# Performance work log

Measured on AMD Instinct MI355X. Metric: run time of the kernel, lower is better.

Reference implementation:

```python
import jax, jax.numpy as jnp
import numpy as np
from jax import lax

B, N, C, FH, FW = 2, 6, 64, 16, 44
D = 64
DEPTH_MIN, DEPTH_MAX = 1.0, 60.0
IMG_H, IMG_W = 256, 704
BEV_H, BEV_W = 128, 128
XMIN, XMAX = -51.2, 51.2
YMIN, YMAX = -51.2, 51.2
BN_EPS = 1e-5


def _make_cameras():
    fx = fy = 557.0
    K = np.array([[fx, 0.0, IMG_W / 2.0], [0.0, fy, IMG_H / 2.0], [0.0, 0.0, 1.0]], np.float32)
    intr = np.broadcast_to(K, (B, N, 3, 3)).copy()
    extr = np.zeros((B, N, 4, 4), np.float32)
    for n in range(N):
        c, s = np.cos(2 * np.pi * n / N), np.sin(2 * np.pi * n / N)
        # columns = [right, down, forward] of camera expressed in ego frame
        Rc = np.array([[s, 0.0, c], [-c, 0.0, s], [0.0, -1.0, 0.0]], np.float32)
        extr[:, n, :3, :3] = Rc
        extr[:, n, :3, 3] = np.array([c, s, 1.5], np.float32)
        extr[:, n, 3, 3] = 1.0
    return jnp.asarray(intr), jnp.asarray(extr)


def _frustum():
    # (D, FH, FW, 3) holding (u*d, v*d, d) in original-image pixel coords
    ds = jnp.linspace(DEPTH_MIN, DEPTH_MAX, D)[:, None, None]
    xs = jnp.linspace(0.0, IMG_W - 1.0, FW)[None, None, :]
    ys = jnp.linspace(0.0, IMG_H - 1.0, FH)[None, :, None]
    d = jnp.broadcast_to(ds, (D, FH, FW))
    x = jnp.broadcast_to(xs, (D, FH, FW))
    y = jnp.broadcast_to(ys, (D, FH, FW))
    return jnp.stack([x * d, y * d, d], axis=-1)


def _conv(x, w, b, pad):
    y = lax.conv_general_dilated(x, w, (1, 1), pad, dimension_numbers=("NCHW", "OIHW", "NCHW"))
    return y + b[None, :, None, None]


def setup_inputs() -> dict:
    key = jax.random.key(0)
    k0, k1, k2 = jax.random.split(key, 3)
    intr, extr = _make_cameras()
    return {
        "features": jax.random.normal(k0, (B, N, C, FH, FW), jnp.float32),
        "intrinsics": intr,
        "extrinsics": extr,
        "conv1_w": jax.random.normal(k1, (C, C, 3, 3), jnp.float32) / np.sqrt(C * 9.0).astype(np.float32),
        "conv1_b": jnp.zeros((C,), jnp.float32),
        "bn_gamma": jnp.ones((C,), jnp.float32),
        "bn_beta": jnp.zeros((C,), jnp.float32),
        "bn_mean": jnp.zeros((C,), jnp.float32),
        "bn_var": jnp.ones((C,), jnp.float32),
        "conv2_w": jax.random.normal(k2, (D, C, 1, 1), jnp.float32) / np.sqrt(float(C)).astype(np.float32),
        "conv2_b": jnp.zeros((D,), jnp.float32),
    }


def reference(features, intrinsics, extrinsics, conv1_w, conv1_b, bn_gamma, bn_beta, bn_mean, bn_var, conv2_w, conv2_b):
    Bv, Nv, Cv, fH, fW = features.shape
    x = features.reshape(Bv * Nv, Cv, fH, fW)

    # DepthNet: conv3x3 -> BN (inference form) -> ReLU -> conv1x1 -> softmax over depth bins
    h = _conv(x, conv1_w, conv1_b, "SAME")
    scale = (bn_gamma / jnp.sqrt(bn_var + BN_EPS))[None, :, None, None]
    h = (h - bn_mean[None, :, None, None]) * scale + bn_beta[None, :, None, None]
    h = jax.nn.relu(h)
    depth = jax.nn.softmax(_conv(h, conv2_w, conv2_b, "VALID"), axis=1)  # (B*N, D, fH, fW)

    # Lift: outer product of features with depth distribution
    volume = x[:, :, None] * depth[:, None]  # (B*N, C, D, fH, fW)

    # Unproject frustum to ego frame for every camera
    pts = _frustum()  # (D, fH, fW, 3)
    Kinv = jnp.linalg.inv(intrinsics)  # (B, N, 3, 3)
    cam = jnp.einsum("bnij,dhwj->bndhwi", Kinv, pts)
    R = extrinsics[..., :3, :3]
    t = extrinsics[..., :3, 3]
    ego = jnp.einsum("bnij,bndhwj->bndhwi", R, cam) + t[:, :, None, None, None, :]

    # BEV voxel indices; invalid points routed to an overflow bucket that is dropped
    ix = jnp.floor((ego[..., 0] - XMIN) / (XMAX - XMIN) * BEV_W).astype(jnp.int32)
    iy = jnp.floor((ego[..., 1] - YMIN) / (YMAX - YMIN) * BEV_H).astype(jnp.int32)
    valid = (ix >= 0) & (ix < BEV_W) & (iy >= 0) & (iy < BEV_H)
    idx = jnp.where(valid, iy * BEV_W + ix, BEV_H * BEV_W)  # (B, N, D, fH, fW)

    # Splat: scatter-add over all cameras/depths/pixels per batch element
    vol = volume.reshape(Bv, Nv, Cv, -1).transpose(0, 2, 1, 3).reshape(Bv, Cv, -1)  # (B, C, N*D*fH*fW)
    idxb = idx.reshape(Bv, -1)

    def pool(v, i):
        return jnp.zeros((Cv, BEV_H * BEV_W + 1), v.dtype).at[:, i].add(v)[:, :-1]

    return jax.vmap(pool)(vol, idxb).reshape(Bv, Cv, BEV_H, BEV_W)
```

## Files before the change

kernel.cpp:

```cpp
#include <hip/hip_runtime.h>
#include <hip/hip_bf16.h>
#include <math.h>

#define B_  2
#define N_  6
#define C_  64
#define FH_ 16
#define FW_ 44
#define D_  64
#define PIX (FH_*FW_)
#define BNI (B_*N_)
#define NPILLAR (BNI*PIX)
#define NPOINT (NPILLAR*D_)
#define BEVH 128
#define BEVW 128
#define BEVC (BEVH*BEVW)
#define NCELL (B_*BEVC)
#define PW 46
#define PP (18*PW)

typedef unsigned int u32;

__device__ __forceinline__ int rlane_i(int v, int l) {
    return __builtin_amdgcn_readlane(v, l);
}
__device__ __forceinline__ float rlane_f(float v, int l) {
    return __int_as_float(__builtin_amdgcn_readlane(__float_as_int(v), l));
}

__global__ __launch_bounds__(256) void k_init_conv(const float* __restrict__ feat,
                                                   const float* __restrict__ w1,
                                                   float* __restrict__ hpAll,
                                                   float* __restrict__ x_t,
                                                   const float* __restrict__ w2,
                                                   float* __restrict__ w2t,
                                                   u32* __restrict__ counts,
                                                   u32* __restrict__ gcursor,
                                                   const float* __restrict__ intr,
                                                   const float* __restrict__ extr,
                                                   double* __restrict__ Mbuf) {
    const int blk = blockIdx.x;
    const int tid = threadIdx.x;

    __shared__ float smem[16 * PP];

    if (blk < 768) {
        if (blk < 128) counts[blk * 256 + tid] = 0u;

        const int bn = blk >> 6;
        const int ch = (blk >> 4) & 3;
        const int o0 = (blk & 15) * 4;
        const int c0 = ch * 16;

        for (int t = tid; t < 4 * PP; t += 256)
            ((float4*)smem)[t] = make_float4(0.f, 0.f, 0.f, 0.f);
        __syncthreads();

        const float4* fb4 = (const float4*)(feat + ((size_t)bn * C_ + c0) * PIX);
#pragma unroll
        for (int k = 0; k < 11; ++k) {
            const int j = k * 256 + tid;
            const int pl = j / 176;
            const int r  = j % 176;
            const int row = r / 11, q = r % 11;
            const float4 v = fb4[j];
            float* dstp = &smem[pl * PP + (row + 1) * PW + q * 4 + 1];
            dstp[0] = v.x; dstp[1] = v.y; dstp[2] = v.z; dstp[3] = v.w;
        }
        __syncthreads();

        const int y0 = tid / FW_,          x0 = tid % FW_;
        const int y1 = (tid + 256) / FW_,  x1 = (tid + 256) % FW_;
        const int y2 = (tid + 512) / FW_,  x2 = (tid + 512) % FW_;
        const int rp0 = y0 * PW + x0;
        const int rp1 = y1 * PW + x1;
        const int rp2 = y2 * PW + x2;

        float a00=0,a01=0,a02=0,a03=0, a10=0,a11=0,a12=0,a13=0,
              a20=0,a21=0,a22=0,a23=0;
#pragma unroll 4
        for (int i = 0; i < 16; ++i) {
            const float* wr0 = w1 + ((size_t)(o0 + 0) * C_ + c0 + i) * 9;
            const float* wr1 = w1 + ((size_t)(o0 + 1) * C_ + c0 + i) * 9;
            const float* wr2 = w1 + ((size_t)(o0 + 2) * C_ + c0 + i) * 9;
            const float* wr3 = w1 + ((size_t)(o0 + 3) * C_ + c0 + i) * 9;
            const float* pb = &smem[i * PP];
#define CONV_SLOT(RP, A0, A1, A2, A3)                                          \
    {                                                                          \
        const float* bb = pb + (RP);                                           \
        const float n0=bb[0], n1=bb[1], n2=bb[2];                              \
        const float n3=bb[PW], n4=bb[PW+1], n5=bb[PW+2];                       \
        const float n6=bb[2*PW], n7=bb[2*PW+1], n8=bb[2*PW+2];                 \
        A0 += n0*wr0[0]+n1*wr0[1]+n2*wr0[2]+n3*wr0[3]+n4*wr0[4]                \
            + n5*wr0[5]+n6*wr0[6]+n7*wr0[7]+n8*wr0[8];                         \
        A1 += n0*wr1[0]+n1*wr1[1]+n2*wr1[2]+n3*wr1[3]+n4*wr1[4]                \
            + n5*wr1[5]+n6*wr1[6]+n7*wr1[7]+n8*wr1[8];                         \
        A2 += n0*wr2[0]+n1*wr2[1]+n2*wr2[2]+n3*wr2[3]+n4*wr2[4]                \
            + n5*wr2[5]+n6*wr2[6]+n7*wr2[7]+n8*wr2[8];                         \
        A3 += n0*wr3[0]+n1*wr3[1]+n2*wr3[2]+n3*wr3[3]+n4*wr3[4]                \
            + n5*wr3[5]+n6*wr3[6]+n7*wr3[7]+n8*wr3[8];                         \
    }
            CONV_SLOT(rp0, a00, a01, a02, a03);
            CONV_SLOT(rp1, a10, a11, a12, a13);
            if (tid < PIX - 512) CONV_SLOT(rp2, a20, a21, a22, a23);
#undef CONV_SLOT
        }
        float* hp = hpAll + (size_t)ch * NPOINT + (size_t)bn * PIX * C_;
        *(float4*)&hp[(size_t)tid * C_ + o0]         = make_float4(a00,a01,a02,a03);
        *(float4*)&hp[(size_t)(tid + 256) * C_ + o0] = make_float4(a10,a11,a12,a13);
        if (tid < PIX - 512)
            *(float4*)&hp[(size_t)(tid + 512) * C_ + o0] = make_float4(a20,a21,a22,a23);
    } else if (blk < 900) {
        const int u  = blk - 768;
        const int bn = u / 11;
        const int p0 = (u % 11) * 64;
        const int lane = tid & 63;
        const int row4 = tid >> 6;
        float* tile = smem;
#pragma unroll
        for (int k = 0; k < 16; ++k) {
            const int c = k * 4 + row4;
            tile[c * 65 + lane] = feat[((size_t)bn * C_ + c) * PIX + p0 + lane];
        }
        __syncthreads();
#pragma unroll
        for (int k = 0; k < 16; ++k) {
            const int r = k * 4 + row4;
            x_t[((size_t)bn * PIX + p0 + r) * C_ + lane] = tile[lane * 65 + r];
        }
    } else {
#pragma unroll
        for (int k = 0; k < 16; ++k) {
            const int idx = k * 256 + tid;
            const int d = idx >> 6, c = idx & 63;
            w2t[c * D_ + d] = w2[idx];
        }
        if (tid == 0) *gcursor = 0u;
        if (tid < BNI) {
            const float* K = &intr[tid * 9];
            const double a00 = K[0], a01 = K[1], a02 = K[2];
            const double a10 = K[3], a11 = K[4], a12 = K[5];
            const double a20 = K[6], a21 = K[7], a22 = K[8];
            const double det = a00 * (a11 * a22 - a12 * a21)
                             - a01 * (a10 * a22 - a12 * a20)
                             + a02 * (a10 * a21 - a11 * a20);
            const double id = 1.0 / det;
            double inv[9];
            inv[0] = (a11 * a22 - a12 * a21) * id;
            inv[1] = (a02 * a21 - a01 * a22) * id;
            inv[2] = (a01 * a12 - a02 * a11) * id;
            inv[3] = (a12 * a20 - a10 * a22) * id;
            inv[4] = (a00 * a22 - a02 * a20) * id;
            inv[5] = (a02 * a10 - a00 * a12) * id;
            inv[6] = (a10 * a21 - a11 * a20) * id;
            inv[7] = (a01 * a20 - a00 * a21) * id;
            inv[8] = (a00 * a11 - a01 * a10) * id;
            const float* E = &extr[tid * 16];
            double* M = &Mbuf[tid * 9];
            for (int r = 0; r < 3; ++r) {
                const double r0 = E[r*4+0], r1 = E[r*4+1], r2 = E[r*4+2];
                M[r*3+0] = r0*inv[0] + r1*inv[3] + r2*inv[6];
                M[r*3+1] = r0*inv[1] + r1*inv[4] + r2*inv[7];
                M[r*3+2] = r0*inv[2] + r1*inv[5] + r2*inv[8];
            }
        }
    }
}

__global__ __launch_bounds__(256) void k_depth(const float* __restrict__ hpAll,
                                               const float* __restrict__ b1,
                                               const float* __restrict__ gma,
                                               const float* __restrict__ bta,
                                               const float* __restrict__ mu,
                                               const float* __restrict__ var,
                                               const float* __restrict__ w2t,
                                               const float* __restrict__ b2,
                                               const double* __restrict__ Mbuf,
                                               const float* __restrict__ extr,
                                               uint2* __restrict__ pc,
                                               u32* __restrict__ counts) {
    const int wv = threadIdx.x >> 6;
    const int d  = threadIdx.x & 63;
    const int pillar = blockIdx.x * 4 + wv;
    const int bn = pillar / PIX;
    const int p  = pillar % PIX;
    const int yi = p / FW_;
    const int xi = p % FW_;

    __shared__ float hs[4][C_];
    {
        const size_t o = (size_t)pillar * C_ + d;
        float h = hpAll[o] + hpAll[NPOINT + o] + hpAll[2 * (size_t)NPOINT + o]
                + hpAll[3 * (size_t)NPOINT + o] + b1[d];
        const float sc = gma[d] / sqrtf(var[d] + 1e-5f);
        h = (h - mu[d]) * sc + bta[d];
        hs[wv][d] = h > 0.f ? h : 0.f;
    }
    __syncthreads();

    float logit = b2[d];
#pragma unroll
    for (int c = 0; c < C_; ++c) logit += hs[wv][c] * w2t[c * D_ + d];

    float m = logit;
#pragma unroll
    for (int off = 32; off; off >>= 1) m = fmaxf(m, __shfl_xor(m, off));
    float e = expf(logit - m);
    float s = e;
#pragma unroll
    for (int off = 32; off; off >>= 1) s += __shfl_xor(s, off);

    const double* M = &Mbuf[bn * 9];
    const double xn = (double)xi * (703.0 / 43.0);
    const double yn = (double)yi * 17.0;
    const double vx = M[0] * xn + M[1] * yn + M[2];
    const double vy = M[3] * xn + M[4] * yn + M[5];
    const double dd = 1.0 + (double)d * (59.0 / 63.0);
    const float* E = &extr[bn * 16];
    const double ex = dd * vx + (double)E[3];
    const double ey = dd * vy + (double)E[7];
    const int ix = (int)floor((ex + 51.2) * 1.25);
    const int iy = (int)floor((ey + 51.2) * 1.25);
    const bool valid = (ix >= 0) && (ix < BEVW) && (iy >= 0) && (iy < BEVH);

    const int i = pillar * D_ + d;
    uint2 rec;
    rec.x = __float_as_uint(e / s);
    if (valid) {
        const int cell = (bn / N_) * BEVC + iy * BEVW + ix;
        const u32 rank = atomicAdd(&counts[cell], 1u);
        rec.y = (rank << 15) | (u32)cell;
    } else {
        rec.y = 0xFFFFFFFFu;
    }
    pc[i] = rec;
}

__global__ __launch_bounds__(256) void k_alloc(const u32* __restrict__ counts,
                                               u32* __restrict__ offs,
                                               u32* __restrict__ gcursor) {
    const int cell = blockIdx.x * 256 + threadIdx.x;
    const int lane = threadIdx.x & 63;
    const u32 len = counts[cell];
    u32 incl = len;
#pragma unroll
    for (int off = 1; off < 64; off <<= 1) {
        u32 t = __shfl_up(incl, off);
        if (lane >= off) incl += t;
    }
    u32 base = 0;
    if (lane == 63) base = atomicAdd(gcursor, incl);
    base = (u32)__shfl((int)base, 63);
    offs[cell] = base + incl - len;
}

__global__ __launch_bounds__(256) void k_zero_place(const uint2* __restrict__ pc,
                                                    const u32* __restrict__ offs,
                                                    const u32* __restrict__ counts,
                                                    const u32* __restrict__ gcursor,
                                                    uint2* __restrict__ sorted,
                                                    u32* __restrict__ offs_end,
                                                    float* __restrict__ spool) {
    const int blk = blockIdx.x;
    const int tid = threadIdx.x;
    if (blk < 2048) {
        const int gt = blk * 256 + tid;
        const int cell = gt >> 4;
        const int q    = gt & 15;
        const u32 n = counts[cell];
        const u32 s = offs[cell];
        const bool needzero = (n == 0u) || ((s >> 6) != ((s + n - 1) >> 6));
        if (needzero)
            *(float4*)&spool[(size_t)cell * C_ + q * 4] =
                make_float4(0.f, 0.f, 0.f, 0.f);
    } else if (blk < 4160) {
        const int i = (blk - 2048) * 256 + tid;
        const uint2 rec = pc[i];
        if (rec.y != 0xFFFFFFFFu) {
            const u32 cell = rec.y & 0x7FFFu;
            const u32 rank = rec.y >> 15;
            const u32 pos  = offs[cell] + rank;
            uint2 o; o.x = rec.x; o.y = (cell << 14) | (u32)(i >> 6);
            sorted[pos] = o;
        }
    } else {
        const u32 total = *gcursor;
        if (tid < 128) {
            uint2 dummy; dummy.x = 0u; dummy.y = 0xFFFFFFFFu;
            sorted[total + tid] = dummy;
        }
        if (tid == 128) *offs_end = total;
    }
}

__global__ __launch_bounds__(256) void k_pool(const uint2* __restrict__ sorted,
                                              const u32* __restrict__ offsets,
                                              const float* __restrict__ x_t,
                                              float* __restrict__ spool) {
    const u32 P = offsets[NCELL];
    const int wv   = threadIdx.x >> 6;
    const int lane = threadIdx.x & 63;
    const u32 j0   = ((u32)blockIdx.x * 4u + (u32)wv) * 64u;
    if (j0 >= P) return;

    const uint2 pr  = sorted[j0 + (u32)lane];
    const float myw = __uint_as_float(pr.x);
    const int mycell = (int)(pr.y >> 14);
    int mypil = (int)(pr.y & 0x3FFFu);
    if (mypil >= NPILLAR) mypil = 0;

    const int prev_cell = (j0 > 0) ? (int)(sorted[j0 - 1].y >> 14) : -1;
    const int next_cell = (int)(sorted[j0 + 64].y >> 14);

    const int upc = __shfl_up(mycell, 1);
    const unsigned long long bm = __ballot(lane == 0 || mycell != upc);

    float xr[8];
#pragma unroll
    for (int t = 0; t < 8; ++t)
        xr[t] = x_t[(size_t)rlane_i(mypil, t) * C_ + lane];

    float acc = 0.f;
    bool first = true;

#pragma unroll
    for (int t = 0; t < 64; ++t) {
        acc += rlane_f(myw, t) * xr[t & 7];
        if (t + 8 < 64)
            xr[t & 7] = x_t[(size_t)rlane_i(mypil, t + 8) * C_ + lane];
        const bool flush = (t == 63) || ((bm >> (t + 1)) & 1ull);
        if (flush) {
            const int cc = rlane_i(mycell, t);
            if (cc < NCELL) {
                float* dst = spool + (size_t)cc * C_ + lane;
                const bool spans = (first && cc == prev_cell)
                                || (t == 63 && next_cell == cc);
                if (spans) atomicAdd(dst, acc);
                else *dst = acc;
            }
            acc = 0.f;
            first = false;
        }
    }
}

__global__ __launch_bounds__(256) void k_out(const float* __restrict__ spool,
                                             float* __restrict__ out) {
    const int tile_i = blockIdx.x;
    const int b  = tile_i >> 8;
    const int c0 = (tile_i & 255) * 64;
    const int tid = threadIdx.x;
    const int lane = tid & 63;
    const int row4 = tid >> 6;

    __shared__ float tile[64][65];
#pragma unroll
    for (int k = 0; k < 16; ++k) {
        const int r = k * 4 + row4;
        tile[r][lane] = spool[((size_t)b * BEVC + c0 + r) * C_ + lane];
    }
    __syncthreads();
#pragma unroll
    for (int k = 0; k < 16; ++k) {
        const int ch = k * 4 + row4;
        out[((size_t)b * C_ + ch) * BEVC + c0 + lane] = tile[lane][ch];
    }
}

extern "C" void kernel_launch(void* const* d_in, const int* in_sizes, int n_in,
                              void* d_out, int out_size, void* d_ws, size_t ws_size,
                              hipStream_t stream) {
    const float* feat  = (const float*)d_in[0];
    const float* intr  = (const float*)d_in[1];
    const float* extr  = (const float*)d_in[2];
    const float* w1    = (const float*)d_in[3];
    const float* b1    = (const float*)d_in[4];
    const float* gma   = (const float*)d_in[5];
    const float* bta   = (const float*)d_in[6];
    const float* mu    = (const float*)d_in[7];
    const float* var   = (const float*)d_in[8];
    const float* w2    = (const float*)d_in[9];
    const float* b2    = (const float*)d_in[10];
    float* out = (float*)d_out;

    double* Mbuf    = (double*)d_ws;
    u32*    gcursor = (u32*)((char*)d_ws + 960);
    uint2*  sorted  = (uint2*)((char*)d_ws + 1024);
    uint2*  pc      = sorted + NPOINT + 128;
    float*  x_t     = (float*)(pc + NPOINT);
    float*  hpAll   = x_t + NPOINT;
    u32*    counts  = (u32*)(hpAll + 4 * (size_t)NPOINT);
    u32*    offs    = counts + NCELL;
    float*  w2t     = (float*)(offs + NCELL + 1);

    float*  spool   = hpAll;

    k_init_conv<<<901, 256, 0, stream>>>(feat, w1, hpAll, x_t, w2, w2t,
                                         counts, gcursor, intr, extr, Mbuf);
    k_depth<<<NPILLAR / 4, 256, 0, stream>>>(hpAll, b1, gma, bta, mu, var,
                                             w2t, b2, Mbuf, extr, pc, counts);
    k_alloc<<<NCELL / 256, 256, 0, stream>>>(counts, offs, gcursor);
    k_zero_place<<<4161, 256, 0, stream>>>(pc, offs, counts, gcursor,
                                           sorted, &offs[NCELL], spool);
    k_pool<<<NPOINT / 64 / 4, 256, 0, stream>>>(sorted, offs, x_t, spool);
    k_out<<<512, 256, 0, stream>>>(spool, out);

    (void)in_sizes; (void)n_in; (void)ws_size; (void)out_size;
}
```

Baseline: 89.31 us.

## Halve conv input-channel split and stage 1x1 weights in LDS with readlane broadcast

The 3x3 conv now uses 2 input-channel chunks of 32 instead of 4 chunks of 16. Each block loops over two 16-channel slabs in shared memory, so it launches half as many blocks and writes half as many partial-sum buffers. The depth kernel sums only 2 partials, copies the 1x1 weights into LDS, and broadcasts activations across the wavefront with readlane instead of going through an LDS round trip. It uses four accumulators for more ILP, and the workspace layout is shrunk to match. The trade-off is fewer, longer conv blocks (384 instead of 768), which lowers parallelism, plus an extra 16KB LDS fill in every depth block.

```diff
diff --git a/kernel.cpp b/kernel.cpp
--- a/kernel.cpp
+++ b/kernel.cpp
@@ -44,29 +44,17 @@
 
     __shared__ float smem[16 * PP];
 
-    if (blk < 768) {
+    if (blk < 384) {
         if (blk < 128) counts[blk * 256 + tid] = 0u;
 
-        const int bn = blk >> 6;
-        const int ch = (blk >> 4) & 3;
-        const int o0 = (blk & 15) * 4;
-        const int c0 = ch * 16;
+        const int bn   = blk >> 5;
+        const int rest = blk & 31;
+        const int ch   = rest >> 4;
+        const int o0   = (rest & 15) * 4;
+        const int c0   = ch * 32;
 
         for (int t = tid; t < 4 * PP; t += 256)
             ((float4*)smem)[t] = make_float4(0.f, 0.f, 0.f, 0.f);
-        __syncthreads();
-
-        const float4* fb4 = (const float4*)(feat + ((size_t)bn * C_ + c0) * PIX);
-#pragma unroll
-        for (int k = 0; k < 11; ++k) {
-            const int j = k * 256 + tid;
-            const int pl = j / 176;
-            const int r  = j % 176;
-            const int row = r / 11, q = r % 11;
-            const float4 v = fb4[j];
-            float* dstp = &smem[pl * PP + (row + 1) * PW + q * 4 + 1];
-            dstp[0] = v.x; dstp[1] = v.y; dstp[2] = v.z; dstp[3] = v.w;
-        }
         __syncthreads();
 
         const int y0 = tid / FW_,          x0 = tid % FW_;
@@ -78,13 +66,31 @@
 
         float a00=0,a01=0,a02=0,a03=0, a10=0,a11=0,a12=0,a13=0,
               a20=0,a21=0,a22=0,a23=0;
+
+#pragma unroll
+        for (int r = 0; r < 2; ++r) {
+            const float4* fb4 =
+                (const float4*)(feat + ((size_t)bn * C_ + c0 + r * 16) * PIX);
+#pragma unroll
+            for (int k = 0; k < 11; ++k) {
+                const int j = k * 256 + tid;
+                const int pl = j / 176;
+                const int rr = j % 176;
+                const int row = rr / 11, q = rr % 11;
+                const float4 v = fb4[j];
+                float* dstp = &smem[pl * PP + (row + 1) * PW + q * 4 + 1];
+                dstp[0] = v.x; dstp[1] = v.y; dstp[2] = v.z; dstp[3] = v.w;
+            }
+            __syncthreads();
+
 #pragma unroll 4
-        for (int i = 0; i < 16; ++i) {
-            const float* wr0 = w1 + ((size_t)(o0 + 0) * C_ + c0 + i) * 9;
-            const float* wr1 = w1 + ((size_t)(o0 + 1) * C_ + c0 + i) * 9;
-            const float* wr2 = w1 + ((size_t)(o0 + 2) * C_ + c0 + i) * 9;
-            const float* wr3 = w1 + ((size_t)(o0 + 3) * C_ + c0 + i) * 9;
-            const float* pb = &smem[i * PP];
+            for (int i = 0; i < 16; ++i) {
+                const int ci = c0 + r * 16 + i;
+                const float* wr0 = w1 + ((size_t)(o0 + 0) * C_ + ci) * 9;
+                const float* wr1 = w1 + ((size_t)(o0 + 1) * C_ + ci) * 9;
+                const float* wr2 = w1 + ((size_t)(o0 + 2) * C_ + ci) * 9;
+                const float* wr3 = w1 + ((size_t)(o0 + 3) * C_ + ci) * 9;
+                const float* pb = &smem[i * PP];
 #define CONV_SLOT(RP, A0, A1, A2, A3)                                          \
     {                                                                          \
         const float* bb = pb + (RP);                                           \
@@ -100,18 +106,21 @@
         A3 += n0*wr3[0]+n1*wr3[1]+n2*wr3[2]+n3*wr3[3]+n4*wr3[4]                \
             + n5*wr3[5]+n6*wr3[6]+n7*wr3[7]+n8*wr3[8];                         \
     }
-            CONV_SLOT(rp0, a00, a01, a02, a03);
-            CONV_SLOT(rp1, a10, a11, a12, a13);
-            if (tid < PIX - 512) CONV_SLOT(rp2, a20, a21, a22, a23);
+                CONV_SLOT(rp0, a00, a01, a02, a03);
+                CONV_SLOT(rp1, a10, a11, a12, a13);
+                if (tid < PIX - 512) CONV_SLOT(rp2, a20, a21, a22, a23);
 #undef CONV_SLOT
-        }
+            }
+            if (r == 0) __syncthreads();
+        }
+
         float* hp = hpAll + (size_t)ch * NPOINT + (size_t)bn * PIX * C_;
         *(float4*)&hp[(size_t)tid * C_ + o0]         = make_float4(a00,a01,a02,a03);
         *(float4*)&hp[(size_t)(tid + 256) * C_ + o0] = make_float4(a10,a11,a12,a13);
         if (tid < PIX - 512)
             *(float4*)&hp[(size_t)(tid + 512) * C_ + o0] = make_float4(a20,a21,a22,a23);
-    } else if (blk < 900) {
-        const int u  = blk - 768;
+    } else if (blk < 516) {
+        const int u  = blk - 384;
         const int bn = u / 11;
         const int p0 = (u % 11) * 64;
         const int lane = tid & 63;
@@ -179,28 +188,39 @@
                                                const float* __restrict__ extr,
                                                uint2* __restrict__ pc,
                                                u32* __restrict__ counts) {
-    const int wv = threadIdx.x >> 6;
-    const int d  = threadIdx.x & 63;
+    const int tid  = threadIdx.x;
+    const int wv   = tid >> 6;
+    const int lane = tid & 63;
     const int pillar = blockIdx.x * 4 + wv;
     const int bn = pillar / PIX;
     const int p  = pillar % PIX;
     const int yi = p / FW_;
     const int xi = p % FW_;
 
-    __shared__ float hs[4][C_];
+    __shared__ float w2s[C_ * D_];
+#pragma unroll
+    for (int k = 0; k < 4; ++k)
+        ((float4*)w2s)[k * 256 + tid] = ((const float4*)w2t)[k * 256 + tid];
+
+    float h;
     {
-        const size_t o = (size_t)pillar * C_ + d;
-        float h = hpAll[o] + hpAll[NPOINT + o] + hpAll[2 * (size_t)NPOINT + o]
-                + hpAll[3 * (size_t)NPOINT + o] + b1[d];
-        const float sc = gma[d] / sqrtf(var[d] + 1e-5f);
-        h = (h - mu[d]) * sc + bta[d];
-        hs[wv][d] = h > 0.f ? h : 0.f;
+        const size_t o = (size_t)pillar * C_ + lane;
+        h = hpAll[o] + hpAll[NPOINT + o] + b1[lane];
+        const float sc = gma[lane] / sqrtf(var[lane] + 1e-5f);
+        h = (h - mu[lane]) * sc + bta[lane];
+        h = h > 0.f ? h : 0.f;
     }
     __syncthreads();
 
-    float logit = b2[d];
-#pragma unroll
-    for (int c = 0; c < C_; ++c) logit += hs[wv][c] * w2t[c * D_ + d];
+    float l0 = 0.f, l1 = 0.f, l2 = 0.f, l3 = 0.f;
+#pragma unroll
+    for (int c = 0; c < C_; c += 4) {
+        l0 += rlane_f(h, c + 0) * w2s[(c + 0) * D_ + lane];
+        l1 += rlane_f(h, c + 1) * w2s[(c + 1) * D_ + lane];
+        l2 += rlane_f(h, c + 2) * w2s[(c + 2) * D_ + lane];
+        l3 += rlane_f(h, c + 3) * w2s[(c + 3) * D_ + lane];
+    }
+    const float logit = b2[lane] + ((l0 + l1) + (l2 + l3));
 
     float m = logit;
 #pragma unroll
@@ -215,7 +235,7 @@
     const double yn = (double)yi * 17.0;
     const double vx = M[0] * xn + M[1] * yn + M[2];
     const double vy = M[3] * xn + M[4] * yn + M[5];
-    const double dd = 1.0 + (double)d * (59.0 / 63.0);
+    const double dd = 1.0 + (double)lane * (59.0 / 63.0);
     const float* E = &extr[bn * 16];
     const double ex = dd * vx + (double)E[3];
     const double ey = dd * vy + (double)E[7];
@@ -223,7 +243,7 @@
     const int iy = (int)floor((ey + 51.2) * 1.25);
     const bool valid = (ix >= 0) && (ix < BEVW) && (iy >= 0) && (iy < BEVH);
 
-    const int i = pillar * D_ + d;
+    const int i = pillar * D_ + lane;
     uint2 rec;
     rec.x = __float_as_uint(e / s);
     if (valid) {
@@ -388,14 +408,14 @@
     uint2*  sorted  = (uint2*)((char*)d_ws + 1024);
     uint2*  pc      = sorted + NPOINT + 128;
     float*  x_t     = (float*)(pc + NPOINT);
-    float*  hpAll   = x_t + NPOINT;
-    u32*    counts  = (u32*)(hpAll + 4 * (size_t)NPOINT);
-    u32*    offs    = counts + NCELL;
-    float*  w2t     = (float*)(offs + NCELL + 1);
-
-    float*  spool   = hpAll;
-
-    k_init_conv<<<901, 256, 0, stream>>>(feat, w1, hpAll, x_t, w2, w2t,
+    float*  region  = x_t + NPOINT;
+    float*  hpAll   = region;
+    float*  spool   = region;
+    u32*    counts  = (u32*)(region + (size_t)NCELL * C_);
+    float*  w2t     = (float*)(counts + NCELL);
+    u32*    offs    = (u32*)(w2t + 4096);
+
+    k_init_conv<<<517, 256, 0, stream>>>(feat, w1, hpAll, x_t, w2, w2t,
                                          counts, gcursor, intr, extr, Mbuf);
     k_depth<<<NPILLAR / 4, 256, 0, stream>>>(hpAll, b1, gma, bta, mu, var,
                                              w2t, b2, Mbuf, extr, pc, counts);
```

New measurement: 97.57 us. 1.09x slower.
